# Performance work log

Hardware: AMD Instinct MI355X
Metric: run time of the kernel (lower is better)

The kernel has to match this reference:

```python
import jax, jax.numpy as jnp
import numpy as np

N_ENT = 50000
N_REL = 16
N_EDGE = 1000000
D = 64


def setup_inputs() -> dict:
    key = jax.random.key(0)
    ks = jax.random.split(key, 20)
    inp = {
        'ent_embed': jax.random.normal(ks[0], (N_ENT, D), jnp.float32) * 0.1,
        'rel_embed': jax.random.normal(ks[1], (N_REL, D), jnp.float32) * 0.1,
        'W_R': jax.random.normal(ks[2], (N_REL, D, D), jnp.float32) * 0.1,
        'W1_0': jax.random.normal(ks[3], (64, 64), jnp.float32) * 0.1,
        'b1_0': jax.random.normal(ks[4], (64,), jnp.float32) * 0.1,
        'W2_0': jax.random.normal(ks[5], (64, 64), jnp.float32) * 0.1,
        'b2_0': jax.random.normal(ks[6], (64,), jnp.float32) * 0.1,
        'W1_1': jax.random.normal(ks[7], (64, 32), jnp.float32) * 0.1,
        'b1_1': jax.random.normal(ks[8], (32,), jnp.float32) * 0.1,
        'W2_1': jax.random.normal(ks[9], (64, 32), jnp.float32) * 0.1,
        'b2_1': jax.random.normal(ks[10], (32,), jnp.float32) * 0.1,
        'W1_2': jax.random.normal(ks[11], (32, 16), jnp.float32) * 0.1,
        'b1_2': jax.random.normal(ks[12], (16,), jnp.float32) * 0.1,
        'W2_2': jax.random.normal(ks[13], (32, 16), jnp.float32) * 0.1,
        'b2_2': jax.random.normal(ks[14], (16,), jnp.float32) * 0.1,
        'src': jax.random.randint(ks[15], (N_EDGE,), 0, N_ENT, jnp.int32),
        'dst': jax.random.randint(ks[16], (N_EDGE,), 0, N_ENT, jnp.int32),
        'etype': jax.random.randint(ks[17], (N_EDGE,), 0, N_REL, jnp.int32),
    }
    return inp


def _l2_normalize(x, eps=1e-12):
    # matches torch F.normalize(p=2, dim=1)
    n = jnp.sqrt(jnp.sum(x * x, axis=1, keepdims=True))
    return x / jnp.maximum(n, eps)


def _kgat_forward(ent_embed, rel_embed, W_R, layer_params, src, dst, etype):
    N = ent_embed.shape[0]
    # --- compute_attention: per-relation TransR projection of all entities ---
    # equivalent to per-edge ent[src] @ W_R[type] without materializing [E, D, D]
    proj = jnp.einsum('nd,rde->rne', ent_embed, W_R)          # [R, N, D]
    r_mul_t = proj[etype, src]                                # [E, D] (tail = src)
    r_mul_h = proj[etype, dst]                                # [E, D] (head = dst)
    att = jnp.sum(r_mul_t * jnp.tanh(r_mul_h + rel_embed[etype]), axis=-1)  # [E]
    # edge softmax grouped by destination node
    m = jax.ops.segment_max(att, dst, num_segments=N)         # [N]
    e = jnp.exp(att - m[dst])
    s = jax.ops.segment_sum(e, dst, num_segments=N)           # [N]
    a = e / s[dst]                                            # [E]

    # --- cf_embedding: bi-interaction aggregator layers ---
    h = ent_embed
    all_embed = [h]
    for (W1, b1, W2, b2) in layer_params:
        msg = a[:, None] * h[src]                             # [E, d_in]
        N_h = jax.ops.segment_sum(msg, dst, num_segments=N)   # [N, d_in]
        out = (jax.nn.leaky_relu((h + N_h) @ W1 + b1, 0.01)
               + jax.nn.leaky_relu((h * N_h) @ W2 + b2, 0.01))
        h = out
        all_embed.append(_l2_normalize(out))
    return jnp.concatenate(all_embed, axis=1)                 # [N, 64+64+32+16=176]


def reference(ent_embed, rel_embed, W_R,
              W1_0, b1_0, W2_0, b2_0,
              W1_1, b1_1, W2_1, b2_1,
              W1_2, b1_2, W2_2, b2_2,
              src, dst, etype):
    layer_params = [(W1_0, b1_0, W2_0, b2_0),
                    (W1_1, b1_1, W2_1, b2_1),
                    (W1_2, b1_2, W2_2, b2_2)]
    return _kgat_forward(ent_embed, rel_embed, W_R, layer_params, src, dst, etype)
```

## Files before the change

kernel.cpp:

```cpp
#include <hip/hip_runtime.h>
#include <hip/hip_bf16.h>
#include <cmath>

#define N_ENT  50000
#define N_RELS 16
#define N_EDGE 1000000
#define DIM    64
#define OUT_STRIDE 176

typedef float f32x4 __attribute__((ext_vector_type(4)));
typedef short s16x8 __attribute__((ext_vector_type(8)));

__device__ inline void bf16x8_unpack(uint4 u, float* f) {
    f[0] = __uint_as_float((u.x & 0xffffu) << 16);
    f[1] = __uint_as_float(u.x & 0xffff0000u);
    f[2] = __uint_as_float((u.y & 0xffffu) << 16);
    f[3] = __uint_as_float(u.y & 0xffff0000u);
    f[4] = __uint_as_float((u.z & 0xffffu) << 16);
    f[5] = __uint_as_float(u.z & 0xffff0000u);
    f[6] = __uint_as_float((u.w & 0xffffu) << 16);
    f[7] = __uint_as_float(u.w & 0xffff0000u);
}

__device__ inline ushort f2bf(float x) {
    __hip_bfloat16 b = __float2bfloat16(x);
    return *(ushort*)&b;
}

__global__ __launch_bounds__(256) void prep_hist_kernel(
        const float* __restrict__ ent,
        ushort* __restrict__ ent_bf,
        ushort* __restrict__ p0, ushort* __restrict__ p1,
        float* __restrict__ out,
        const int* __restrict__ dst, int* __restrict__ counts,
        int* __restrict__ off) {
    int i = blockIdx.x * blockDim.x + threadIdx.x;
    if (i < N_ENT * DIM) {
        float v = ent[i];
        ushort b = f2bf(v);
        int n = i >> 6, c = i & 63;
        ent_bf[i] = b;
        if (c < 32) p0[n * 32 + c] = b;
        else        p1[n * 32 + (c - 32)] = b;
        out[(size_t)n * OUT_STRIDE + c] = v;
    }
    if (i < N_EDGE) off[i] = atomicAdd(&counts[dst[i]], 1);
}

__global__ __launch_bounds__(256) void scan1_kernel(
        const int* __restrict__ counts, int* __restrict__ excl,
        int* __restrict__ bsum, int n) {
    __shared__ int sh[256];
    int t = threadIdx.x;
    int i = blockIdx.x * 256 + t;
    int c = (i < n) ? counts[i] : 0;
    sh[t] = c;
    __syncthreads();
    for (int off = 1; off < 256; off <<= 1) {
        int v = (t >= off) ? sh[t - off] : 0;
        __syncthreads();
        sh[t] += v;
        __syncthreads();
    }
    if (i < n) excl[i] = sh[t] - c;
    if (t == 255) bsum[blockIdx.x] = sh[255];
}

__global__ __launch_bounds__(256) void scan2_kernel(
        const int* __restrict__ bsum, int* __restrict__ boff,
        int* __restrict__ row_ptr, int nb, int n) {
    __shared__ int sh[256];
    int t = threadIdx.x;
    int v = (t < nb) ? bsum[t] : 0;
    sh[t] = v;
    __syncthreads();
    for (int off = 1; off < 256; off <<= 1) {
        int x = (t >= off) ? sh[t - off] : 0;
        __syncthreads();
        sh[t] += x;
        __syncthreads();
    }
    if (t < nb) boff[t] = sh[t] - v;
    if (t == nb - 1) row_ptr[n] = sh[t];
}

__global__ __launch_bounds__(256) void scan3_pos_kernel(
        const int* __restrict__ excl, const int* __restrict__ boff,
        int* __restrict__ row_ptr,
        const int* __restrict__ src, const int* __restrict__ dst,
        const int* __restrict__ etype, const int* __restrict__ off,
        unsigned long long* __restrict__ einfo) {
    int i = blockIdx.x * blockDim.x + threadIdx.x;
    if (i < N_ENT) row_ptr[i] = excl[i] + boff[i >> 8];
    if (i < N_EDGE) {
        int d = dst[i];
        int pos = excl[d] + boff[d >> 8] + off[i];
        unsigned long long info =
              (unsigned long long)(unsigned)src[i]
            | ((unsigned long long)(unsigned)d << 16)
            | ((unsigned long long)(unsigned)etype[i] << 32)
            | ((unsigned long long)(unsigned)pos << 36);
        einfo[i] = info;
    }
}

__global__ __launch_bounds__(256) void gz_mfma_kernel(
        const ushort* __restrict__ ent_bf,
        const float*  __restrict__ W_R,
        const float*  __restrict__ rel,
        __hip_bfloat16* __restrict__ Z) {
    __shared__ float lds[4][16 * 68 + 16];
    int lane = threadIdx.x & 63;
    int wv   = threadIdx.x >> 6;
    int m    = lane & 15;
    int q    = lane >> 4;
    int r    = blockIdx.y;
    int wid  = blockIdx.x * 4 + wv;
    int nw   = gridDim.x * 4;

    const float* Wr = W_R + (size_t)r * DIM * DIM;
    s16x8 b1[4][2], b2[4][2];
#pragma unroll
    for (int c = 0; c < 4; ++c)
#pragma unroll
        for (int ch = 0; ch < 2; ++ch)
#pragma unroll
            for (int j = 0; j < 8; ++j) {
                b1[c][ch][j] = (short)f2bf(Wr[(ch * 32 + q * 8 + j) * DIM + c * 16 + m]);
                b2[c][ch][j] = (short)f2bf(Wr[(c * 16 + m) * DIM + ch * 32 + q * 8 + j]);
            }
    float relv[4];
#pragma unroll
    for (int c = 0; c < 4; ++c) relv[c] = rel[r * DIM + c * 16 + m];

    float* myLds = lds[wv];
    const int ntiles = N_ENT / 16;

    for (int t = wid; t < ntiles; t += nw) {
        int row0 = t * 16;
        const s16x8* arow = (const s16x8*)(ent_bf + (size_t)(row0 + m) * DIM);
        s16x8 a0 = arow[q];
        s16x8 a1 = arow[4 + q];
        f32x4 acc[4];
#pragma unroll
        for (int c = 0; c < 4; ++c) acc[c] = (f32x4){0.f, 0.f, 0.f, 0.f};
#pragma unroll
        for (int c = 0; c < 4; ++c) {
            acc[c] = __builtin_amdgcn_mfma_f32_16x16x32_bf16(a0, b1[c][0], acc[c], 0, 0, 0);
            acc[c] = __builtin_amdgcn_mfma_f32_16x16x32_bf16(a1, b1[c][1], acc[c], 0, 0, 0);
        }
#pragma unroll
        for (int c = 0; c < 4; ++c)
#pragma unroll
            for (int i = 0; i < 4; ++i) {
                float x = acc[c][i] + relv[c];
                float g = 1.f - 2.f / (__expf(2.f * x) + 1.f);
                myLds[(q * 4 + i) * 68 + c * 16 + m] = g;
            }
        s16x8 a2[2];
#pragma unroll
        for (int ch = 0; ch < 2; ++ch)
#pragma unroll
            for (int j = 0; j < 8; ++j)
                a2[ch][j] = (short)f2bf(myLds[m * 68 + ch * 32 + q * 8 + j]);

        f32x4 zacc[4];
#pragma unroll
        for (int c = 0; c < 4; ++c) zacc[c] = (f32x4){0.f, 0.f, 0.f, 0.f};
#pragma unroll
        for (int c = 0; c < 4; ++c) {
            zacc[c] = __builtin_amdgcn_mfma_f32_16x16x32_bf16(a2[0], b2[c][0], zacc[c], 0, 0, 0);
            zacc[c] = __builtin_amdgcn_mfma_f32_16x16x32_bf16(a2[1], b2[c][1], zacc[c], 0, 0, 0);
        }
        __hip_bfloat16* zrow = Z + ((size_t)r * N_ENT + row0) * DIM;
#pragma unroll
        for (int c = 0; c < 4; ++c)
#pragma unroll
            for (int i = 0; i < 4; ++i)
                zrow[(q * 4 + i) * DIM + c * 16 + m] = __float2bfloat16(zacc[c][i]);
    }
}

__global__ __launch_bounds__(256) void att_dot_kernel(
        const ushort* __restrict__ ent_bf,
        const __hip_bfloat16* __restrict__ Z,
        const unsigned long long* __restrict__ einfo,
        uint2* __restrict__ es_csr,
        int n_edge) {
    int tid  = blockIdx.x * blockDim.x + threadIdx.x;
    int lane = threadIdx.x & 63;
    int sub  = lane >> 3;
    int q    = lane & 7;
    int base = (tid >> 6) * 16;
    int e0 = base + sub;
    int e1 = base + 8 + sub;
    if (e0 >= n_edge) return;
    bool v1 = (e1 < n_edge);
    unsigned long long i0 = einfo[e0];
    unsigned long long i1 = v1 ? einfo[e1] : i0;

    int s0 = (int)(i0 & 0xffffu);
    int d0 = (int)((i0 >> 16) & 0xffffu);
    int r0 = (int)((i0 >> 32) & 0xfu);
    int p0 = (int)(i0 >> 36);
    int s1 = (int)(i1 & 0xffffu);
    int d1 = (int)((i1 >> 16) & 0xffffu);
    int r1 = (int)((i1 >> 32) & 0xfu);
    int p1 = (int)(i1 >> 36);

    uint4 uz0 = *(const uint4*)(Z + ((size_t)r0 * N_ENT + d0) * DIM + q * 8);
    uint4 ue0 = *(const uint4*)(ent_bf + (size_t)s0 * DIM + q * 8);
    uint4 uz1 = *(const uint4*)(Z + ((size_t)r1 * N_ENT + d1) * DIM + q * 8);
    uint4 ue1 = *(const uint4*)(ent_bf + (size_t)s1 * DIM + q * 8);

    float z0[8], w0[8], z1[8], w1[8];
    bf16x8_unpack(uz0, z0);
    bf16x8_unpack(ue0, w0);
    bf16x8_unpack(uz1, z1);
    bf16x8_unpack(ue1, w1);

    float pr0 = 0.f, pr1 = 0.f;
#pragma unroll
    for (int j = 0; j < 8; ++j) {
        pr0 = fmaf(w0[j], z0[j], pr0);
        pr1 = fmaf(w1[j], z1[j], pr1);
    }
    pr0 += __shfl_xor(pr0, 1, 64);
    pr1 += __shfl_xor(pr1, 1, 64);
    pr0 += __shfl_xor(pr0, 2, 64);
    pr1 += __shfl_xor(pr1, 2, 64);
    pr0 += __shfl_xor(pr0, 4, 64);
    pr1 += __shfl_xor(pr1, 4, 64);

    if (q == 0) {
        es_csr[p0] = make_uint2(__float_as_uint(pr0), (unsigned)s0);
        if (v1) es_csr[p1] = make_uint2(__float_as_uint(pr1), (unsigned)s1);
    }
}

__global__ __launch_bounds__(256) void softmax_kernel(
        const int* __restrict__ row_ptr, uint2* __restrict__ es_csr,
        float* __restrict__ inv_sum, int n_node) {
    int wid  = (blockIdx.x * blockDim.x + threadIdx.x) >> 6;
    int lane = threadIdx.x & 63;
    if (wid >= n_node) return;
    int start = row_ptr[wid], end = row_ptr[wid + 1];

    float m = -INFINITY;
    for (int i = start + lane; i < end; i += 64)
        m = fmaxf(m, __uint_as_float(es_csr[i].x));
#pragma unroll
    for (int off = 32; off > 0; off >>= 1)
        m = fmaxf(m, __shfl_xor(m, off, 64));

    float ssum = 0.f;
    for (int i = start + lane; i < end; i += 64) {
        float e = expf(__uint_as_float(es_csr[i].x) - m);
        es_csr[i].x = __float_as_uint(e);
        ssum += e;
    }
#pragma unroll
    for (int off = 32; off > 0; off >>= 1)
        ssum += __shfl_xor(ssum, off, 64);

    if (lane == 0)
        inv_sum[wid] = (end > start) ? (1.0f / ssum) : 0.f;
}

__global__ __launch_bounds__(256) void agg_kernel(
        const ushort* __restrict__ plane,
        const uint2* __restrict__ es_csr,
        const int* __restrict__ row_ptr,
        const float* __restrict__ inv_sum,
        float* __restrict__ N_h, int stride, int off, int n_node) {
    int wid  = (blockIdx.x * blockDim.x + threadIdx.x) >> 6;
    int lane = threadIdx.x & 63;
    if (wid >= n_node) return;
    int q   = lane & 3;
    int sub = lane >> 2;

    int start = row_ptr[wid], end = row_ptr[wid + 1];
    float inv = inv_sum[wid];
    float acc[8];
#pragma unroll
    for (int j = 0; j < 8; ++j) acc[j] = 0.f;

    for (int p = start + sub; p < end; p += 16) {
        uint2 es = es_csr[p];
        float av = __uint_as_float(es.x);
        int   si = (int)es.y;
        uint4 u  = *(const uint4*)(plane + (size_t)si * 32 + q * 8);
        float g[8];
        bf16x8_unpack(u, g);
#pragma unroll
        for (int j = 0; j < 8; ++j) acc[j] = fmaf(av, g[j], acc[j]);
    }
#pragma unroll
    for (int mask = 4; mask < 64; mask <<= 1)
#pragma unroll
        for (int j = 0; j < 8; ++j)
            acc[j] += __shfl_xor(acc[j], mask, 64);

    if (sub == 0) {
        float* dstp = N_h + (size_t)wid * stride + off + q * 8;
        *(float4*)(dstp)     = (float4){acc[0] * inv, acc[1] * inv, acc[2] * inv, acc[3] * inv};
        *(float4*)(dstp + 4) = (float4){acc[4] * inv, acc[5] * inv, acc[6] * inv, acc[7] * inv};
    }
}

template <int D_IN, int D_OUT>
__global__ __launch_bounds__(256) void mlp_mfma_kernel(
        const ushort* __restrict__ h_p0,
        const ushort* __restrict__ h_p1,
        const float* __restrict__ N_h,
        const float* __restrict__ W1, const float* __restrict__ b1,
        const float* __restrict__ W2, const float* __restrict__ b2,
        ushort* __restrict__ ho_p0,
        ushort* __restrict__ ho_p1,
        float* __restrict__ out_buf, int out_col) {
    constexpr int CH = D_IN / 32;
    constexpr int CT = D_OUT / 16;

    int lane = threadIdx.x & 63;
    int m    = lane & 15;
    int q    = lane >> 4;
    int wid  = blockIdx.x * (blockDim.x >> 6) + (threadIdx.x >> 6);
    int nw   = gridDim.x * (blockDim.x >> 6);

    s16x8 bu[CT][CH], bv[CT][CH];
#pragma unroll
    for (int c = 0; c < CT; ++c)
#pragma unroll
        for (int ch = 0; ch < CH; ++ch)
#pragma unroll
            for (int j = 0; j < 8; ++j) {
                int k = ch * 32 + q * 8 + j;
                bu[c][ch][j] = (short)f2bf(W1[k * D_OUT + c * 16 + m]);
                bv[c][ch][j] = (short)f2bf(W2[k * D_OUT + c * 16 + m]);
            }

    const int ntiles = N_ENT / 16;
    for (int t = wid; t < ntiles; t += nw) {
        int row0 = t * 16;
        s16x8 au[CH], av[CH];
#pragma unroll
        for (int ch = 0; ch < CH; ++ch) {
            const ushort* hp = (ch == 0) ? h_p0 : h_p1;
            uint4 hu = *(const uint4*)(hp + (size_t)(row0 + m) * 32 + q * 8);
            float hv8[8];
            bf16x8_unpack(hu, hv8);
            const float4* np = (const float4*)(N_h + (size_t)(row0 + m) * D_IN + ch * 32 + q * 8);
            float4 na = np[0], nb = np[1];
            float nv[8] = {na.x, na.y, na.z, na.w, nb.x, nb.y, nb.z, nb.w};
#pragma unroll
            for (int j = 0; j < 8; ++j) {
                au[ch][j] = (short)f2bf(hv8[j] + nv[j]);
                av[ch][j] = (short)f2bf(hv8[j] * nv[j]);
            }
        }

        f32x4 accu[CT], accv[CT];
#pragma unroll
        for (int c = 0; c < CT; ++c) {
            accu[c] = (f32x4){0.f, 0.f, 0.f, 0.f};
            accv[c] = (f32x4){0.f, 0.f, 0.f, 0.f};
        }
#pragma unroll
        for (int c = 0; c < CT; ++c)
#pragma unroll
            for (int ch = 0; ch < CH; ++ch) {
                accu[c] = __builtin_amdgcn_mfma_f32_16x16x32_bf16(au[ch], bu[c][ch], accu[c], 0, 0, 0);
                accv[c] = __builtin_amdgcn_mfma_f32_16x16x32_bf16(av[ch], bv[c][ch], accv[c], 0, 0, 0);
            }

        float res[CT][4];
        float sq[4] = {0.f, 0.f, 0.f, 0.f};
#pragma unroll
        for (int c = 0; c < CT; ++c) {
            float bb1 = b1[c * 16 + m];
            float bb2 = b2[c * 16 + m];
#pragma unroll
            for (int i = 0; i < 4; ++i) {
                float o1 = accu[c][i] + bb1;
                float o2 = accv[c][i] + bb2;
                float r1 = (o1 >= 0.f) ? o1 : 0.01f * o1;
                float r2 = (o2 >= 0.f) ? o2 : 0.01f * o2;
                float rr = r1 + r2;
                res[c][i] = rr;
                sq[i] = fmaf(rr, rr, sq[i]);
            }
        }
#pragma unroll
        for (int mask = 1; mask < 16; mask <<= 1)
#pragma unroll
            for (int i = 0; i < 4; ++i)
                sq[i] += __shfl_xor(sq[i], mask, 64);

#pragma unroll
        for (int i = 0; i < 4; ++i) {
            int row = row0 + q * 4 + i;
            float inv = 1.f / fmaxf(sqrtf(sq[i]), 1e-12f);
#pragma unroll
            for (int c = 0; c < CT; ++c) {
                int col = c * 16 + m;
                out_buf[(size_t)row * OUT_STRIDE + out_col + col] = res[c][i] * inv;
                if (ho_p0) {
                    ushort hb = f2bf(res[c][i]);
                    if (col < 32) ho_p0[(size_t)row * 32 + col] = hb;
                    else          ho_p1[(size_t)row * 32 + (col - 32)] = hb;
                }
            }
        }
    }
}

extern "C" void kernel_launch(void* const* d_in, const int* in_sizes, int n_in,
                              void* d_out, int out_size, void* d_ws, size_t ws_size,
                              hipStream_t stream) {
    const float* ent  = (const float*)d_in[0];
    const float* rel  = (const float*)d_in[1];
    const float* W_R  = (const float*)d_in[2];
    const float* W1_0 = (const float*)d_in[3];
    const float* b1_0 = (const float*)d_in[4];
    const float* W2_0 = (const float*)d_in[5];
    const float* b2_0 = (const float*)d_in[6];
    const float* W1_1 = (const float*)d_in[7];
    const float* b1_1 = (const float*)d_in[8];
    const float* W2_1 = (const float*)d_in[9];
    const float* b2_1 = (const float*)d_in[10];
    const float* W1_2 = (const float*)d_in[11];
    const float* b1_2 = (const float*)d_in[12];
    const float* W2_2 = (const float*)d_in[13];
    const float* b2_2 = (const float*)d_in[14];
    const int*   src   = (const int*)d_in[15];
    const int*   dst   = (const int*)d_in[16];
    const int*   etype = (const int*)d_in[17];
    float* out = (float*)d_out;

    char* w = (char*)d_ws;
    uint2*  es_csr  = (uint2*)w;  w += (size_t)N_EDGE * 8;
    int*    counts  = (int*)w;    w += (size_t)(N_ENT + 64) * 4;
    int*    row_ptr = (int*)w;    w += (size_t)(N_ENT + 64) * 4;
    float*  inv_sum = (float*)w;  w += (size_t)(N_ENT + 64) * 4;
    int*    excl    = (int*)w;    w += (size_t)(N_ENT + 64) * 4;
    int*    bsum    = (int*)w;    w += 256 * 4;
    int*    boff    = (int*)w;    w += 256 * 4;
    ushort* ent_bf  = (ushort*)w; w += (size_t)N_ENT * 64 * 2;
    ushort* ent_p0  = (ushort*)w; w += (size_t)N_ENT * 32 * 2;
    ushort* ent_p1  = (ushort*)w; w += (size_t)N_ENT * 32 * 2;
    ushort* h1_p0   = (ushort*)w; w += (size_t)N_ENT * 32 * 2;
    ushort* h1_p1   = (ushort*)w; w += (size_t)N_ENT * 32 * 2;
    ushort* h2      = (ushort*)w; w += (size_t)N_ENT * 32 * 2;
    float*  N_h     = (float*)w;  w += (size_t)N_ENT * 64 * 4;
    __hip_bfloat16* Z = (__hip_bfloat16*)w;
    (void)ws_size;

    int* off = (int*)Z;
    unsigned long long* einfo = (unsigned long long*)N_h;

    hipMemsetAsync(counts, 0, (size_t)N_ENT * 4, stream);

    const int nb = (N_ENT + 255) / 256;

    prep_hist_kernel<<<(N_ENT * DIM + 255) / 256, 256, 0, stream>>>(
        ent, ent_bf, ent_p0, ent_p1, out, dst, counts, off);
    scan1_kernel<<<nb, 256, 0, stream>>>(counts, excl, bsum, N_ENT);
    scan2_kernel<<<1, 256, 0, stream>>>(bsum, boff, row_ptr, nb, N_ENT);
    scan3_pos_kernel<<<(N_EDGE + 255) / 256, 256, 0, stream>>>(
        excl, boff, row_ptr, src, dst, etype, off, einfo);

    gz_mfma_kernel<<<dim3(64, N_RELS), 256, 0, stream>>>(ent_bf, W_R, rel, Z);
    att_dot_kernel<<<(N_EDGE / 16 * 64 + 255) / 256, 256, 0, stream>>>(
        ent_bf, Z, einfo, es_csr, N_EDGE);

    softmax_kernel<<<(N_ENT + 3) / 4, 256, 0, stream>>>(row_ptr, es_csr, inv_sum, N_ENT);

    const int aggGrid = (N_ENT + 3) / 4;
    const int mlpGrid = 782;

    agg_kernel<<<aggGrid, 256, 0, stream>>>(ent_p0, es_csr, row_ptr, inv_sum, N_h, 64, 0,  N_ENT);
    agg_kernel<<<aggGrid, 256, 0, stream>>>(ent_p1, es_csr, row_ptr, inv_sum, N_h, 64, 32, N_ENT);
    mlp_mfma_kernel<64, 64><<<mlpGrid, 256, 0, stream>>>(
        ent_p0, ent_p1, N_h, W1_0, b1_0, W2_0, b2_0, h1_p0, h1_p1, out, 64);

    agg_kernel<<<aggGrid, 256, 0, stream>>>(h1_p0, es_csr, row_ptr, inv_sum, N_h, 64, 0,  N_ENT);
    agg_kernel<<<aggGrid, 256, 0, stream>>>(h1_p1, es_csr, row_ptr, inv_sum, N_h, 64, 32, N_ENT);
    mlp_mfma_kernel<64, 32><<<mlpGrid, 256, 0, stream>>>(
        h1_p0, h1_p1, N_h, W1_1, b1_1, W2_1, b2_1, h2, nullptr, out, 128);

    agg_kernel<<<aggGrid, 256, 0, stream>>>(h2, es_csr, row_ptr, inv_sum, N_h, 32, 0, N_ENT);
    mlp_mfma_kernel<32, 16><<<mlpGrid, 256, 0, stream>>>(
        h2, nullptr, N_h, W1_2, b1_2, W2_2, b2_2, nullptr, nullptr, out, 160);
}
```

Measured before the change: 412.9 us.

## Use permuted interleaved bf16 entity layout, fuse aggregation planes, recompute softmax exp

Replaces the split 32-column planes with a single permuted 64-wide bf16 table, compensating by permuting weight rows, so each layer-0/1 aggregation is one kernel instead of two. The softmax pass no longer writes exponentials back and stores only max and inverse sum; the aggregation kernels recompute the exponential per edge. The Z store in the projection kernel is packed into 16-byte writes using lane shuffles and packed bf16 conversion, and its grid is widened. This trades extra exp work in three aggregation passes for fewer launches, fewer scattered stores and less edge-array write traffic, at the cost of fragile index permutations.

```diff
diff --git a/kernel.cpp b/kernel.cpp
--- a/kernel.cpp
+++ b/kernel.cpp
@@ -27,10 +27,21 @@
     return *(ushort*)&b;
 }
 
+__device__ inline uint cvt_pk_bf16(float lo, float hi) {
+    uint r;
+    asm("v_cvt_pk_bf16_f32 %0, %1, %2" : "=v"(r) : "v"(lo), "v"(hi));
+    return r;
+}
+
+__device__ __host__ inline int pcol(int p) {
+    int qp = (p >> 3) & 7;
+    int k  = p & 7;
+    return 16 * (k >> 1) + 2 * qp + (k & 1);
+}
+
 __global__ __launch_bounds__(256) void prep_hist_kernel(
         const float* __restrict__ ent,
-        ushort* __restrict__ ent_bf,
-        ushort* __restrict__ p0, ushort* __restrict__ p1,
+        ushort* __restrict__ ent_pi,
         float* __restrict__ out,
         const int* __restrict__ dst, int* __restrict__ counts,
         int* __restrict__ off) {
@@ -39,9 +50,8 @@
         float v = ent[i];
         ushort b = f2bf(v);
         int n = i >> 6, c = i & 63;
-        ent_bf[i] = b;
-        if (c < 32) p0[n * 32 + c] = b;
-        else        p1[n * 32 + (c - 32)] = b;
+        int pos = ((c & 15) >> 1) * 8 + ((c >> 4) << 1) + (c & 1);
+        ent_pi[(size_t)n * 64 + pos] = b;
         out[(size_t)n * OUT_STRIDE + c] = v;
     }
     if (i < N_EDGE) off[i] = atomicAdd(&counts[dst[i]], 1);
@@ -105,11 +115,11 @@
 }
 
 __global__ __launch_bounds__(256) void gz_mfma_kernel(
-        const ushort* __restrict__ ent_bf,
+        const ushort* __restrict__ ent_pi,
         const float*  __restrict__ W_R,
         const float*  __restrict__ rel,
-        __hip_bfloat16* __restrict__ Z) {
-    __shared__ float lds[4][16 * 68 + 16];
+        ushort* __restrict__ Z) {
+    __shared__ __align__(16) float lds[4][16 * 68 + 16];
     int lane = threadIdx.x & 63;
     int wv   = threadIdx.x >> 6;
     int m    = lane & 15;
@@ -126,7 +136,7 @@
         for (int ch = 0; ch < 2; ++ch)
 #pragma unroll
             for (int j = 0; j < 8; ++j) {
-                b1[c][ch][j] = (short)f2bf(Wr[(ch * 32 + q * 8 + j) * DIM + c * 16 + m]);
+                b1[c][ch][j] = (short)f2bf(Wr[pcol(ch * 32 + q * 8 + j) * DIM + c * 16 + m]);
                 b2[c][ch][j] = (short)f2bf(Wr[(c * 16 + m) * DIM + ch * 32 + q * 8 + j]);
             }
     float relv[4];
@@ -138,7 +148,7 @@
 
     for (int t = wid; t < ntiles; t += nw) {
         int row0 = t * 16;
-        const s16x8* arow = (const s16x8*)(ent_bf + (size_t)(row0 + m) * DIM);
+        const s16x8* arow = (const s16x8*)(ent_pi + (size_t)(row0 + m) * DIM);
         s16x8 a0 = arow[q];
         s16x8 a1 = arow[4 + q];
         f32x4 acc[4];
@@ -157,33 +167,62 @@
                 float g = 1.f - 2.f / (__expf(2.f * x) + 1.f);
                 myLds[(q * 4 + i) * 68 + c * 16 + m] = g;
             }
-        s16x8 a2[2];
-#pragma unroll
-        for (int ch = 0; ch < 2; ++ch)
-#pragma unroll
-            for (int j = 0; j < 8; ++j)
-                a2[ch][j] = (short)f2bf(myLds[m * 68 + ch * 32 + q * 8 + j]);
+        union { uint u[4]; s16x8 v; } a2u[2];
+#pragma unroll
+        for (int ch = 0; ch < 2; ++ch) {
+            const f32x4* gp = (const f32x4*)(myLds + m * 68 + ch * 32 + q * 8);
+            f32x4 g0 = gp[0];
+            f32x4 g1 = gp[1];
+            a2u[ch].u[0] = cvt_pk_bf16(g0[0], g0[1]);
+            a2u[ch].u[1] = cvt_pk_bf16(g0[2], g0[3]);
+            a2u[ch].u[2] = cvt_pk_bf16(g1[0], g1[1]);
+            a2u[ch].u[3] = cvt_pk_bf16(g1[2], g1[3]);
+        }
 
         f32x4 zacc[4];
 #pragma unroll
         for (int c = 0; c < 4; ++c) zacc[c] = (f32x4){0.f, 0.f, 0.f, 0.f};
 #pragma unroll
         for (int c = 0; c < 4; ++c) {
-            zacc[c] = __builtin_amdgcn_mfma_f32_16x16x32_bf16(a2[0], b2[c][0], zacc[c], 0, 0, 0);
-            zacc[c] = __builtin_amdgcn_mfma_f32_16x16x32_bf16(a2[1], b2[c][1], zacc[c], 0, 0, 0);
-        }
-        __hip_bfloat16* zrow = Z + ((size_t)r * N_ENT + row0) * DIM;
+            zacc[c] = __builtin_amdgcn_mfma_f32_16x16x32_bf16(a2u[0].v, b2[c][0], zacc[c], 0, 0, 0);
+            zacc[c] = __builtin_amdgcn_mfma_f32_16x16x32_bf16(a2u[1].v, b2[c][1], zacc[c], 0, 0, 0);
+        }
+
+        float oth[4][4];
 #pragma unroll
         for (int c = 0; c < 4; ++c)
 #pragma unroll
             for (int i = 0; i < 4; ++i)
-                zrow[(q * 4 + i) * DIM + c * 16 + m] = __float2bfloat16(zacc[c][i]);
+                oth[c][i] = __shfl_xor(zacc[c][i], 1, 64);
+        int par = m & 1;
+        uint wrd[4][4];
+#pragma unroll
+        for (int c = 0; c < 4; ++c)
+#pragma unroll
+            for (int i = 0; i < 4; ++i) {
+                float lo = par ? oth[c][i] : zacc[c][i];
+                float hi = par ? zacc[c][i] : oth[c][i];
+                wrd[c][i] = cvt_pk_bf16(lo, hi);
+            }
+        uint4 W0, W1;
+        ((uint*)&W0)[0] = par ? wrd[0][2] : wrd[0][0];
+        ((uint*)&W0)[1] = par ? wrd[1][2] : wrd[1][0];
+        ((uint*)&W0)[2] = par ? wrd[2][2] : wrd[2][0];
+        ((uint*)&W0)[3] = par ? wrd[3][2] : wrd[3][0];
+        ((uint*)&W1)[0] = par ? wrd[0][3] : wrd[0][1];
+        ((uint*)&W1)[1] = par ? wrd[1][3] : wrd[1][1];
+        ((uint*)&W1)[2] = par ? wrd[2][3] : wrd[2][1];
+        ((uint*)&W1)[3] = par ? wrd[3][3] : wrd[3][1];
+        int rowA = row0 + 4 * q + (par ? 2 : 0);
+        ushort* zb = Z + ((size_t)r * N_ENT + rowA) * 64 + (m >> 1) * 8;
+        *(uint4*)zb = W0;
+        *(uint4*)(zb + 64) = W1;
     }
 }
 
 __global__ __launch_bounds__(256) void att_dot_kernel(
-        const ushort* __restrict__ ent_bf,
-        const __hip_bfloat16* __restrict__ Z,
+        const ushort* __restrict__ ent_pi,
+        const ushort* __restrict__ Z,
         const unsigned long long* __restrict__ einfo,
         uint2* __restrict__ es_csr,
         int n_edge) {
@@ -209,9 +248,9 @@
     int p1 = (int)(i1 >> 36);
 
     uint4 uz0 = *(const uint4*)(Z + ((size_t)r0 * N_ENT + d0) * DIM + q * 8);
-    uint4 ue0 = *(const uint4*)(ent_bf + (size_t)s0 * DIM + q * 8);
+    uint4 ue0 = *(const uint4*)(ent_pi + (size_t)s0 * DIM + q * 8);
     uint4 uz1 = *(const uint4*)(Z + ((size_t)r1 * N_ENT + d1) * DIM + q * 8);
-    uint4 ue1 = *(const uint4*)(ent_bf + (size_t)s1 * DIM + q * 8);
+    uint4 ue1 = *(const uint4*)(ent_pi + (size_t)s1 * DIM + q * 8);
 
     float z0[8], w0[8], z1[8], w1[8];
     bf16x8_unpack(uz0, z0);
@@ -238,9 +277,9 @@
     }
 }
 
-__global__ __launch_bounds__(256) void softmax_kernel(
-        const int* __restrict__ row_ptr, uint2* __restrict__ es_csr,
-        float* __restrict__ inv_sum, int n_node) {
+__global__ __launch_bounds__(256) void stats_kernel(
+        const int* __restrict__ row_ptr, const uint2* __restrict__ es_csr,
+        float2* __restrict__ stats, int n_node) {
     int wid  = (blockIdx.x * blockDim.x + threadIdx.x) >> 6;
     int lane = threadIdx.x & 63;
     if (wid >= n_node) return;
@@ -254,25 +293,64 @@
         m = fmaxf(m, __shfl_xor(m, off, 64));
 
     float ssum = 0.f;
-    for (int i = start + lane; i < end; i += 64) {
-        float e = expf(__uint_as_float(es_csr[i].x) - m);
-        es_csr[i].x = __float_as_uint(e);
-        ssum += e;
-    }
+    for (int i = start + lane; i < end; i += 64)
+        ssum += __expf(__uint_as_float(es_csr[i].x) - m);
 #pragma unroll
     for (int off = 32; off > 0; off >>= 1)
         ssum += __shfl_xor(ssum, off, 64);
 
     if (lane == 0)
-        inv_sum[wid] = (end > start) ? (1.0f / ssum) : 0.f;
-}
-
-__global__ __launch_bounds__(256) void agg_kernel(
-        const ushort* __restrict__ plane,
+        stats[wid] = make_float2(m, (end > start) ? (1.0f / ssum) : 0.f);
+}
+
+__global__ __launch_bounds__(256) void agg64_kernel(
+        const ushort* __restrict__ tab,
         const uint2* __restrict__ es_csr,
         const int* __restrict__ row_ptr,
-        const float* __restrict__ inv_sum,
-        float* __restrict__ N_h, int stride, int off, int n_node) {
+        const float2* __restrict__ stats,
+        float* __restrict__ N_h, int n_node) {
+    int wid  = (blockIdx.x * blockDim.x + threadIdx.x) >> 6;
+    int lane = threadIdx.x & 63;
+    if (wid >= n_node) return;
+    int q   = lane & 7;
+    int sub = lane >> 3;
+
+    int start = row_ptr[wid], end = row_ptr[wid + 1];
+    float2 st = stats[wid];
+    float mx = st.x, inv = st.y;
+    float acc[8];
+#pragma unroll
+    for (int j = 0; j < 8; ++j) acc[j] = 0.f;
+
+    for (int p = start + sub; p < end; p += 8) {
+        uint2 es = es_csr[p];
+        float av = __expf(__uint_as_float(es.x) - mx);
+        int   si = (int)es.y;
+        uint4 u  = *(const uint4*)(tab + (size_t)si * 64 + q * 8);
+        float g[8];
+        bf16x8_unpack(u, g);
+#pragma unroll
+        for (int j = 0; j < 8; ++j) acc[j] = fmaf(av, g[j], acc[j]);
+    }
+#pragma unroll
+    for (int mask = 8; mask < 64; mask <<= 1)
+#pragma unroll
+        for (int j = 0; j < 8; ++j)
+            acc[j] += __shfl_xor(acc[j], mask, 64);
+
+    if (sub == 0) {
+        float* dstp = N_h + (size_t)wid * 64 + q * 8;
+        *(float4*)(dstp)     = (float4){acc[0] * inv, acc[1] * inv, acc[2] * inv, acc[3] * inv};
+        *(float4*)(dstp + 4) = (float4){acc[4] * inv, acc[5] * inv, acc[6] * inv, acc[7] * inv};
+    }
+}
+
+__global__ __launch_bounds__(256) void agg32_kernel(
+        const ushort* __restrict__ tab,
+        const uint2* __restrict__ es_csr,
+        const int* __restrict__ row_ptr,
+        const float2* __restrict__ stats,
+        float* __restrict__ N_h, int n_node) {
     int wid  = (blockIdx.x * blockDim.x + threadIdx.x) >> 6;
     int lane = threadIdx.x & 63;
     if (wid >= n_node) return;
@@ -280,16 +358,17 @@
     int sub = lane >> 2;
 
     int start = row_ptr[wid], end = row_ptr[wid + 1];
-    float inv = inv_sum[wid];
+    float2 st = stats[wid];
+    float mx = st.x, inv = st.y;
     float acc[8];
 #pragma unroll
     for (int j = 0; j < 8; ++j) acc[j] = 0.f;
 
     for (int p = start + sub; p < end; p += 16) {
         uint2 es = es_csr[p];
-        float av = __uint_as_float(es.x);
+        float av = __expf(__uint_as_float(es.x) - mx);
         int   si = (int)es.y;
-        uint4 u  = *(const uint4*)(plane + (size_t)si * 32 + q * 8);
+        uint4 u  = *(const uint4*)(tab + (size_t)si * 32 + q * 8);
         float g[8];
         bf16x8_unpack(u, g);
 #pragma unroll
@@ -302,21 +381,19 @@
             acc[j] += __shfl_xor(acc[j], mask, 64);
 
     if (sub == 0) {
-        float* dstp = N_h + (size_t)wid * stride + off + q * 8;
+        float* dstp = N_h + (size_t)wid * 32 + q * 8;
         *(float4*)(dstp)     = (float4){acc[0] * inv, acc[1] * inv, acc[2] * inv, acc[3] * inv};
         *(float4*)(dstp + 4) = (float4){acc[4] * inv, acc[5] * inv, acc[6] * inv, acc[7] * inv};
     }
 }
 
-template <int D_IN, int D_OUT>
+template <int D_IN, int D_OUT, bool PERM>
 __global__ __launch_bounds__(256) void mlp_mfma_kernel(
-        const ushort* __restrict__ h_p0,
-        const ushort* __restrict__ h_p1,
+        const ushort* __restrict__ h,
         const float* __restrict__ N_h,
         const float* __restrict__ W1, const float* __restrict__ b1,
         const float* __restrict__ W2, const float* __restrict__ b2,
-        ushort* __restrict__ ho_p0,
-        ushort* __restrict__ ho_p1,
+        ushort* __restrict__ ho,
         float* __restrict__ out_buf, int out_col) {
     constexpr int CH = D_IN / 32;
     constexpr int CT = D_OUT / 16;
@@ -334,7 +411,8 @@
         for (int ch = 0; ch < CH; ++ch)
 #pragma unroll
             for (int j = 0; j < 8; ++j) {
-                int k = ch * 32 + q * 8 + j;
+                int p = ch * 32 + q * 8 + j;
+                int k = PERM ? pcol(p) : p;
                 bu[c][ch][j] = (short)f2bf(W1[k * D_OUT + c * 16 + m]);
                 bv[c][ch][j] = (short)f2bf(W2[k * D_OUT + c * 16 + m]);
             }
@@ -345,8 +423,7 @@
         s16x8 au[CH], av[CH];
 #pragma unroll
         for (int ch = 0; ch < CH; ++ch) {
-            const ushort* hp = (ch == 0) ? h_p0 : h_p1;
-            uint4 hu = *(const uint4*)(hp + (size_t)(row0 + m) * 32 + q * 8);
+            uint4 hu = *(const uint4*)(h + (size_t)(row0 + m) * D_IN + ch * 32 + q * 8);
             float hv8[8];
             bf16x8_unpack(hu, hv8);
             const float4* np = (const float4*)(N_h + (size_t)(row0 + m) * D_IN + ch * 32 + q * 8);
@@ -404,11 +481,7 @@
             for (int c = 0; c < CT; ++c) {
                 int col = c * 16 + m;
                 out_buf[(size_t)row * OUT_STRIDE + out_col + col] = res[c][i] * inv;
-                if (ho_p0) {
-                    ushort hb = f2bf(res[c][i]);
-                    if (col < 32) ho_p0[(size_t)row * 32 + col] = hb;
-                    else          ho_p1[(size_t)row * 32 + (col - 32)] = hb;
-                }
+                if (ho) ho[(size_t)row * D_OUT + col] = f2bf(res[c][i]);
             }
         }
     }
@@ -441,18 +514,15 @@
     uint2*  es_csr  = (uint2*)w;  w += (size_t)N_EDGE * 8;
     int*    counts  = (int*)w;    w += (size_t)(N_ENT + 64) * 4;
     int*    row_ptr = (int*)w;    w += (size_t)(N_ENT + 64) * 4;
-    float*  inv_sum = (float*)w;  w += (size_t)(N_ENT + 64) * 4;
+    float2* stats   = (float2*)w; w += (size_t)(N_ENT + 64) * 8;
     int*    excl    = (int*)w;    w += (size_t)(N_ENT + 64) * 4;
     int*    bsum    = (int*)w;    w += 256 * 4;
     int*    boff    = (int*)w;    w += 256 * 4;
-    ushort* ent_bf  = (ushort*)w; w += (size_t)N_ENT * 64 * 2;
-    ushort* ent_p0  = (ushort*)w; w += (size_t)N_ENT * 32 * 2;
-    ushort* ent_p1  = (ushort*)w; w += (size_t)N_ENT * 32 * 2;
-    ushort* h1_p0   = (ushort*)w; w += (size_t)N_ENT * 32 * 2;
-    ushort* h1_p1   = (ushort*)w; w += (size_t)N_ENT * 32 * 2;
+    ushort* ent_pi  = (ushort*)w; w += (size_t)N_ENT * 64 * 2;
+    ushort* h1      = (ushort*)w; w += (size_t)N_ENT * 64 * 2;
     ushort* h2      = (ushort*)w; w += (size_t)N_ENT * 32 * 2;
     float*  N_h     = (float*)w;  w += (size_t)N_ENT * 64 * 4;
-    __hip_bfloat16* Z = (__hip_bfloat16*)w;
+    ushort* Z       = (ushort*)w;
     (void)ws_size;
 
     int* off = (int*)Z;
@@ -463,32 +533,30 @@
     const int nb = (N_ENT + 255) / 256;
 
     prep_hist_kernel<<<(N_ENT * DIM + 255) / 256, 256, 0, stream>>>(
-        ent, ent_bf, ent_p0, ent_p1, out, dst, counts, off);
+        ent, ent_pi, out, dst, counts, off);
     scan1_kernel<<<nb, 256, 0, stream>>>(counts, excl, bsum, N_ENT);
     scan2_kernel<<<1, 256, 0, stream>>>(bsum, boff, row_ptr, nb, N_ENT);
     scan3_pos_kernel<<<(N_EDGE + 255) / 256, 256, 0, stream>>>(
         excl, boff, row_ptr, src, dst, etype, off, einfo);
 
-    gz_mfma_kernel<<<dim3(64, N_RELS), 256, 0, stream>>>(ent_bf, W_R, rel, Z);
+    gz_mfma_kernel<<<dim3(96, N_RELS), 256, 0, stream>>>(ent_pi, W_R, rel, Z);
     att_dot_kernel<<<(N_EDGE / 16 * 64 + 255) / 256, 256, 0, stream>>>(
-        ent_bf, Z, einfo, es_csr, N_EDGE);
-
-    softmax_kernel<<<(N_ENT + 3) / 4, 256, 0, stream>>>(row_ptr, es_csr, inv_sum, N_ENT);
+        ent_pi, Z, einfo, es_csr, N_EDGE);
+
+    stats_kernel<<<(N_ENT + 3) / 4, 256, 0, stream>>>(row_ptr, es_csr, stats, N_ENT);
 
     const int aggGrid = (N_ENT + 3) / 4;
     const int mlpGrid = 782;
 
-    agg_kernel<<<aggGrid, 256, 0, stream>>>(ent_p0, es_csr, row_ptr, inv_sum, N_h, 64, 0,  N_ENT);
-    agg_kernel<<<aggGrid, 256, 0, stream>>>(ent_p1, es_csr, row_ptr, inv_sum, N_h, 64, 32, N_ENT);
-    mlp_mfma_kernel<64, 64><<<mlpGrid, 256, 0, stream>>>(
-        ent_p0, ent_p1, N_h, W1_0, b1_0, W2_0, b2_0, h1_p0, h1_p1, out, 64);
-
-    agg_kernel<<<aggGrid, 256, 0, stream>>>(h1_p0, es_csr, row_ptr, inv_sum, N_h, 64, 0,  N_ENT);
-    agg_kernel<<<aggGrid, 256, 0, stream>>>(h1_p1, es_csr, row_ptr, inv_sum, N_h, 64, 32, N_ENT);
-    mlp_mfma_kernel<64, 32><<<mlpGrid, 256, 0, stream>>>(
-        h1_p0, h1_p1, N_h, W1_1, b1_1, W2_1, b2_1, h2, nullptr, out, 128);
-
-    agg_kernel<<<aggGrid, 256, 0, stream>>>(h2, es_csr, row_ptr, inv_sum, N_h, 32, 0, N_ENT);
-    mlp_mfma_kernel<32, 16><<<mlpGrid, 256, 0, stream>>>(
-        h2, nullptr, N_h, W1_2, b1_2, W2_2, b2_2, nullptr, nullptr, out, 160);
-}
+    agg64_kernel<<<aggGrid, 256, 0, stream>>>(ent_pi, es_csr, row_ptr, stats, N_h, N_ENT);
+    mlp_mfma_kernel<64, 64, true><<<mlpGrid, 256, 0, stream>>>(
+        ent_pi, N_h, W1_0, b1_0, W2_0, b2_0, h1, out, 64);
+
+    agg64_kernel<<<aggGrid, 256, 0, stream>>>(h1, es_csr, row_ptr, stats, N_h, N_ENT);
+    mlp_mfma_kernel<64, 32, false><<<mlpGrid, 256, 0, stream>>>(
+        h1, N_h, W1_1, b1_1, W2_1, b2_1, h2, out, 128);
+
+    agg32_kernel<<<aggGrid, 256, 0, stream>>>(h2, es_csr, row_ptr, stats, N_h, N_ENT);
+    mlp_mfma_kernel<32, 16, false><<<mlpGrid, 256, 0, stream>>>(
+        h2, N_h, W1_2, b1_2, W2_2, b2_2, nullptr, out, 160);
+}
```

New measurement: 416.9 us. No clear change (+1.0%).
